# Kernel tuning notes

Measured on AMD Instinct MI355X. Metric: run time of the kernel, lower is better.

Reference implementation:

```python
import jax, jax.numpy as jnp
import numpy as np

N = 100000      # nodes
DEG = 16        # fixed degree
E = N * DEG     # edges
C_IN = 128
C_OUT = 128


def setup_inputs() -> dict:
    key = jax.random.key(0)
    k1, k2, k3, k4, k5 = jax.random.split(key, 5)
    x = jax.random.normal(k1, (N, C_IN), dtype=jnp.float32)
    # glorot-ish init for the dense weight
    scale = jnp.sqrt(6.0 / (C_IN + C_OUT)).astype(jnp.float32)
    weight = jax.random.uniform(k2, (C_IN, C_OUT), dtype=jnp.float32, minval=-1.0, maxval=1.0) * scale
    bias = jax.random.normal(k3, (C_OUT,), dtype=jnp.float32) * 0.02
    # fixed-degree CSR: every node has DEG in-edges; CSC analogously
    rowptr = (jnp.arange(N + 1, dtype=jnp.int32) * DEG)
    colind = jax.random.randint(k4, (E,), 0, N, dtype=jnp.int32)
    colptr = (jnp.arange(N + 1, dtype=jnp.int32) * DEG)
    rowind = jax.random.randint(k5, (E,), 0, N, dtype=jnp.int32)
    return {"x": x, "weight": weight, "bias": bias,
            "rowptr": rowptr, "colind": colind,
            "colptr": colptr, "rowind": rowind}


def _deg_inv_sqrt(indptr, dtype):
    deg = (indptr[1:] - indptr[:-1]).astype(dtype)
    return (1.0 / jnp.sqrt(deg))[:, None]  # [N, 1]


def reference(x, weight, bias, rowptr, colind, colptr, rowind):
    # dense transform: [N, C_in] @ [C_in, C_out]
    h = x @ weight
    in_norm = _deg_inv_sqrt(rowptr, h.dtype)    # 1/sqrt(in-degree)
    out_norm = _deg_inv_sqrt(colptr, h.dtype)   # 1/sqrt(out-degree)
    h = h * out_norm
    # CSR SpMM (unweighted): out[i] = sum_{e in [rowptr[i], rowptr[i+1])} h[colind[e]]
    n_nodes = rowptr.shape[0] - 1
    n_edges = colind.shape[0]
    row = jnp.searchsorted(rowptr, jnp.arange(n_edges, dtype=rowptr.dtype), side="right") - 1
    aggr = jax.ops.segment_sum(h[colind], row, num_segments=n_nodes)
    aggr = aggr * in_norm + bias
    return aggr
```

## Files before the change

### kernel.cpp

```cpp
#include <hip/hip_runtime.h>
#include <hip/hip_bf16.h>

#define N_NODES 100000
#define DEG 16
#define C 128
#define LDS_STRIDE 136

typedef __attribute__((ext_vector_type(8))) short short8;
typedef __attribute__((ext_vector_type(4))) float f32x4;

__device__ inline unsigned short f2bf(float f) {
    unsigned int u = __builtin_bit_cast(unsigned int, f);
    u += 0x7fffu + ((u >> 16) & 1u);
    return (unsigned short)(u >> 16);
}
__device__ inline float bflo(unsigned int p) { return __builtin_bit_cast(float, p << 16); }
__device__ inline float bfhi(unsigned int p) { return __builtin_bit_cast(float, p & 0xffff0000u); }

__global__ __launch_bounds__(256, 4)
void gcn_gemm_kernel(const float* __restrict__ x, const float* __restrict__ w,
                     const int* __restrict__ colptr, unsigned short* __restrict__ h)
{
    __shared__ unsigned short wt[C * LDS_STRIDE];

    int tid = threadIdx.x;
    for (int i = tid; i < C * C; i += 256) {
        int k = i >> 7;
        int n = i & 127;
        wt[n * LDS_STRIDE + k] = f2bf(w[i]);
    }
    __syncthreads();

    int wave = tid >> 6;
    int lane = tid & 63;
    int tile = blockIdx.x * 4 + wave;
    int m0 = tile * 16;
    if (m0 >= N_NODES) return;

    int lrow = lane & 15;
    int quad = lane >> 4;

    int gm_a = m0 + lrow;
    const float* xrow = x + (long)gm_a * C;
    short8 afrag[4];
#pragma unroll
    for (int kc = 0; kc < 4; ++kc) {
        int k0 = kc * 32 + quad * 8;
        f32x4 x0 = *reinterpret_cast<const f32x4*>(xrow + k0);
        f32x4 x1 = *reinterpret_cast<const f32x4*>(xrow + k0 + 4);
        short8 a;
        a[0] = (short)f2bf(x0[0]); a[1] = (short)f2bf(x0[1]);
        a[2] = (short)f2bf(x0[2]); a[3] = (short)f2bf(x0[3]);
        a[4] = (short)f2bf(x1[0]); a[5] = (short)f2bf(x1[1]);
        a[6] = (short)f2bf(x1[2]); a[7] = (short)f2bf(x1[3]);
        afrag[kc] = a;
    }

    float onorm[4];
#pragma unroll
    for (int r = 0; r < 4; ++r) {
        int gm = m0 + quad * 4 + r;
        onorm[r] = rsqrtf((float)(colptr[gm + 1] - colptr[gm]));
    }

#pragma unroll
    for (int nt = 0; nt < 8; ++nt) {
        f32x4 acc = {0.f, 0.f, 0.f, 0.f};
        int n = nt * 16 + lrow;
#pragma unroll
        for (int kc = 0; kc < 4; ++kc) {
            int k0 = kc * 32 + quad * 8;
            short8 b = *reinterpret_cast<const short8*>(&wt[n * LDS_STRIDE + k0]);
            acc = __builtin_amdgcn_mfma_f32_16x16x32_bf16(afrag[kc], b, acc, 0, 0, 0);
        }
#pragma unroll
        for (int r = 0; r < 4; ++r) {
            int gm = m0 + quad * 4 + r;
            h[(long)gm * C + nt * 16 + lrow] = f2bf(acc[r] * onorm[r]);
        }
    }
}

__global__ __launch_bounds__(256, 8)
void gcn_aggr_kernel(const unsigned short* __restrict__ h,
                     const int* __restrict__ rowptr,
                     const int* __restrict__ colind,
                     const float* __restrict__ bias,
                     float* __restrict__ out)
{
    int tid = threadIdx.x;
    int wave = tid >> 6;
    int lane = tid & 63;
    int node = blockIdx.x * 4 + wave;

    int cg = lane & 15;
    int eg = lane >> 4;

    int base = rowptr[node];
    int deg  = rowptr[node + 1] - base;
    float innorm = rsqrtf((float)deg);

    int myidx = colind[base + cg];

    float acc[8];
#pragma unroll
    for (int i = 0; i < 8; ++i) acc[i] = 0.f;

#pragma unroll
    for (int it = 0; it < 4; ++it) {
        int e = it * 4 + eg;
        int j = __shfl(myidx, e);
        const unsigned short* row = h + (long)j * C + cg * 8;
        int4 v = *reinterpret_cast<const int4*>(row);
        unsigned int p0 = (unsigned int)v.x;
        unsigned int p1 = (unsigned int)v.y;
        unsigned int p2 = (unsigned int)v.z;
        unsigned int p3 = (unsigned int)v.w;
        acc[0] += bflo(p0); acc[1] += bfhi(p0);
        acc[2] += bflo(p1); acc[3] += bfhi(p1);
        acc[4] += bflo(p2); acc[5] += bfhi(p2);
        acc[6] += bflo(p3); acc[7] += bfhi(p3);
    }

#pragma unroll
    for (int i = 0; i < 8; ++i) {
        acc[i] += __shfl_xor(acc[i], 16);
        acc[i] += __shfl_xor(acc[i], 32);
    }

    if (eg == 0) {
        const f32x4* bp = reinterpret_cast<const f32x4*>(bias + cg * 8);
        f32x4 b0 = bp[0], b1 = bp[1];
        f32x4 o0, o1;
        o0[0] = acc[0] * innorm + b0[0];
        o0[1] = acc[1] * innorm + b0[1];
        o0[2] = acc[2] * innorm + b0[2];
        o0[3] = acc[3] * innorm + b0[3];
        o1[0] = acc[4] * innorm + b1[0];
        o1[1] = acc[5] * innorm + b1[1];
        o1[2] = acc[6] * innorm + b1[2];
        o1[3] = acc[7] * innorm + b1[3];
        float* op = out + (long)node * C + cg * 8;
        *reinterpret_cast<f32x4*>(op)     = o0;
        *reinterpret_cast<f32x4*>(op + 4) = o1;
    }
}

extern "C" void kernel_launch(void* const* d_in, const int* in_sizes, int n_in,
                              void* d_out, int out_size, void* d_ws, size_t ws_size,
                              hipStream_t stream) {
    const float* x      = (const float*)d_in[0];
    const float* w      = (const float*)d_in[1];
    const float* bias   = (const float*)d_in[2];
    const int*   rowptr = (const int*)d_in[3];
    const int*   colind = (const int*)d_in[4];
    const int*   colptr = (const int*)d_in[5];
    float* out = (float*)d_out;
    unsigned short* h = (unsigned short*)d_ws;

    gcn_gemm_kernel<<<1563, 256, 0, stream>>>(x, w, colptr, h);
    gcn_aggr_kernel<<<25000, 256, 0, stream>>>(h, rowptr, colind, bias, out);
}
```

Baseline: 175.9 us.

## Make GEMM persistent with register-resident weights and prefetch; batch two nodes per aggregation wave

The GEMM kernel becomes persistent: 256 blocks of 8 waves. Each block stores W in LDS in MFMA-fragment order, and each wave keeps all B fragments in registers. Every wave loops over row tiles and prefetches the next tile's x while doing the MFMAs on the current one. This removes the per-block weight conversion that the old version repeated across 1563 blocks, and overlaps loads with compute, at the cost of high register pressure (128 VGPRs for the B fragments). The aggregation kernel now handles two nodes per wave and issues all 8 gather loads before accumulating, to raise memory-level parallelism. Its launch-bounds occupancy hint drops from 8 to 6.

Result: no change. 174.6 us (-0.7%).

```diff
diff --git a/kernel.cpp b/kernel.cpp
--- a/kernel.cpp
+++ b/kernel.cpp
@@ -4,7 +4,9 @@
 #define N_NODES 100000
 #define DEG 16
 #define C 128
-#define LDS_STRIDE 136
+#define NTILES 6250
+#define GEMM_BLOCKS 256
+#define GEMM_WAVES 8
 
 typedef __attribute__((ext_vector_type(8))) short short8;
 typedef __attribute__((ext_vector_type(4))) float f32x4;
@@ -17,71 +19,95 @@
 __device__ inline float bflo(unsigned int p) { return __builtin_bit_cast(float, p << 16); }
 __device__ inline float bfhi(unsigned int p) { return __builtin_bit_cast(float, p & 0xffff0000u); }
 
-__global__ __launch_bounds__(256, 4)
+__global__ __launch_bounds__(512, 2)
 void gcn_gemm_kernel(const float* __restrict__ x, const float* __restrict__ w,
                      const int* __restrict__ colptr, unsigned short* __restrict__ h)
 {
-    __shared__ unsigned short wt[C * LDS_STRIDE];
+    __shared__ unsigned short wfrag[32 * 64 * 8];
 
     int tid = threadIdx.x;
-    for (int i = tid; i < C * C; i += 256) {
-        int k = i >> 7;
-        int n = i & 127;
-        wt[n * LDS_STRIDE + k] = f2bf(w[i]);
+    for (int i = tid; i < C * C; i += 512) {
+        int k = i >> 7, n = i & 127;
+        int nt = n >> 4, lr = n & 15;
+        int kc = k >> 5, quad = (k >> 3) & 3, j = k & 7;
+        wfrag[((((nt << 2) + kc) << 6) + (quad << 4) + lr) * 8 + j] = f2bf(w[i]);
     }
     __syncthreads();
 
     int wave = tid >> 6;
     int lane = tid & 63;
-    int tile = blockIdx.x * 4 + wave;
-    int m0 = tile * 16;
-    if (m0 >= N_NODES) return;
-
     int lrow = lane & 15;
     int quad = lane >> 4;
 
-    int gm_a = m0 + lrow;
-    const float* xrow = x + (long)gm_a * C;
-    short8 afrag[4];
-#pragma unroll
-    for (int kc = 0; kc < 4; ++kc) {
-        int k0 = kc * 32 + quad * 8;
-        f32x4 x0 = *reinterpret_cast<const f32x4*>(xrow + k0);
-        f32x4 x1 = *reinterpret_cast<const f32x4*>(xrow + k0 + 4);
-        short8 a;
-        a[0] = (short)f2bf(x0[0]); a[1] = (short)f2bf(x0[1]);
-        a[2] = (short)f2bf(x0[2]); a[3] = (short)f2bf(x0[3]);
-        a[4] = (short)f2bf(x1[0]); a[5] = (short)f2bf(x1[1]);
-        a[6] = (short)f2bf(x1[2]); a[7] = (short)f2bf(x1[3]);
-        afrag[kc] = a;
-    }
-
-    float onorm[4];
-#pragma unroll
-    for (int r = 0; r < 4; ++r) {
-        int gm = m0 + quad * 4 + r;
-        onorm[r] = rsqrtf((float)(colptr[gm + 1] - colptr[gm]));
-    }
-
-#pragma unroll
-    for (int nt = 0; nt < 8; ++nt) {
-        f32x4 acc = {0.f, 0.f, 0.f, 0.f};
-        int n = nt * 16 + lrow;
+    short8 bf[8][4];
+#pragma unroll
+    for (int nt = 0; nt < 8; ++nt)
+#pragma unroll
+        for (int kc = 0; kc < 4; ++kc)
+            bf[nt][kc] = *reinterpret_cast<const short8*>(
+                &wfrag[((((nt << 2) + kc) << 6) + lane) * 8]);
+
+    int tile = blockIdx.x * GEMM_WAVES + wave;
+    if (tile >= NTILES) return;
+    const int tstride = GEMM_BLOCKS * GEMM_WAVES;
+
+    f32x4 xb[8];
+    {
+        const float* xr = x + (long)(tile * 16 + lrow) * C + quad * 8;
 #pragma unroll
         for (int kc = 0; kc < 4; ++kc) {
-            int k0 = kc * 32 + quad * 8;
-            short8 b = *reinterpret_cast<const short8*>(&wt[n * LDS_STRIDE + k0]);
-            acc = __builtin_amdgcn_mfma_f32_16x16x32_bf16(afrag[kc], b, acc, 0, 0, 0);
-        }
+            xb[2*kc]   = *reinterpret_cast<const f32x4*>(xr + kc * 32);
+            xb[2*kc+1] = *reinterpret_cast<const f32x4*>(xr + kc * 32 + 4);
+        }
+    }
+
+    while (true) {
+        int m0 = tile * 16;
+        short8 af[4];
+#pragma unroll
+        for (int kc = 0; kc < 4; ++kc) {
+            short8 a;
+            a[0] = (short)f2bf(xb[2*kc][0]);   a[1] = (short)f2bf(xb[2*kc][1]);
+            a[2] = (short)f2bf(xb[2*kc][2]);   a[3] = (short)f2bf(xb[2*kc][3]);
+            a[4] = (short)f2bf(xb[2*kc+1][0]); a[5] = (short)f2bf(xb[2*kc+1][1]);
+            a[6] = (short)f2bf(xb[2*kc+1][2]); a[7] = (short)f2bf(xb[2*kc+1][3]);
+            af[kc] = a;
+        }
+        float onorm[4];
 #pragma unroll
         for (int r = 0; r < 4; ++r) {
             int gm = m0 + quad * 4 + r;
-            h[(long)gm * C + nt * 16 + lrow] = f2bf(acc[r] * onorm[r]);
-        }
-    }
-}
-
-__global__ __launch_bounds__(256, 8)
+            onorm[r] = rsqrtf((float)(colptr[gm + 1] - colptr[gm]));
+        }
+
+        int next = tile + tstride;
+        bool more = next < NTILES;
+        if (more) {
+            const float* xr = x + (long)(next * 16 + lrow) * C + quad * 8;
+#pragma unroll
+            for (int kc = 0; kc < 4; ++kc) {
+                xb[2*kc]   = *reinterpret_cast<const f32x4*>(xr + kc * 32);
+                xb[2*kc+1] = *reinterpret_cast<const f32x4*>(xr + kc * 32 + 4);
+            }
+        }
+
+#pragma unroll
+        for (int nt = 0; nt < 8; ++nt) {
+            f32x4 acc = {0.f, 0.f, 0.f, 0.f};
+#pragma unroll
+            for (int kc = 0; kc < 4; ++kc)
+                acc = __builtin_amdgcn_mfma_f32_16x16x32_bf16(af[kc], bf[nt][kc], acc, 0, 0, 0);
+            unsigned short* hp = h + (long)(m0 + quad * 4) * C + nt * 16 + lrow;
+#pragma unroll
+            for (int r = 0; r < 4; ++r)
+                hp[r * C] = f2bf(acc[r] * onorm[r]);
+        }
+        if (!more) break;
+        tile = next;
+    }
+}
+
+__global__ __launch_bounds__(256, 6)
 void gcn_aggr_kernel(const unsigned short* __restrict__ h,
                      const int* __restrict__ rowptr,
                      const int* __restrict__ colind,
@@ -91,56 +117,73 @@
     int tid = threadIdx.x;
     int wave = tid >> 6;
     int lane = tid & 63;
-    int node = blockIdx.x * 4 + wave;
+    int node0 = (blockIdx.x * 4 + wave) * 2;
+    int node1 = node0 + 1;
 
     int cg = lane & 15;
     int eg = lane >> 4;
 
-    int base = rowptr[node];
-    int deg  = rowptr[node + 1] - base;
-    float innorm = rsqrtf((float)deg);
-
-    int myidx = colind[base + cg];
-
-    float acc[8];
-#pragma unroll
-    for (int i = 0; i < 8; ++i) acc[i] = 0.f;
-
+    int base0 = rowptr[node0];
+    int deg0  = rowptr[node0 + 1] - base0;
+    int base1 = rowptr[node1];
+    int deg1  = rowptr[node1 + 1] - base1;
+    float innorm0 = rsqrtf((float)deg0);
+    float innorm1 = rsqrtf((float)deg1);
+
+    int myidx0 = colind[base0 + cg];
+    int myidx1 = colind[base1 + cg];
+
+    int4 v0[4], v1[4];
 #pragma unroll
     for (int it = 0; it < 4; ++it) {
         int e = it * 4 + eg;
-        int j = __shfl(myidx, e);
-        const unsigned short* row = h + (long)j * C + cg * 8;
-        int4 v = *reinterpret_cast<const int4*>(row);
-        unsigned int p0 = (unsigned int)v.x;
-        unsigned int p1 = (unsigned int)v.y;
-        unsigned int p2 = (unsigned int)v.z;
-        unsigned int p3 = (unsigned int)v.w;
-        acc[0] += bflo(p0); acc[1] += bfhi(p0);
-        acc[2] += bflo(p1); acc[3] += bfhi(p1);
-        acc[4] += bflo(p2); acc[5] += bfhi(p2);
-        acc[6] += bflo(p3); acc[7] += bfhi(p3);
+        int j0 = __shfl(myidx0, e);
+        int j1 = __shfl(myidx1, e);
+        v0[it] = *reinterpret_cast<const int4*>(h + (long)j0 * C + cg * 8);
+        v1[it] = *reinterpret_cast<const int4*>(h + (long)j1 * C + cg * 8);
+    }
+
+    float acc0[8], acc1[8];
+#pragma unroll
+    for (int i = 0; i < 8; ++i) { acc0[i] = 0.f; acc1[i] = 0.f; }
+
+#pragma unroll
+    for (int it = 0; it < 4; ++it) {
+        unsigned int p;
+        p = (unsigned int)v0[it].x; acc0[0] += bflo(p); acc0[1] += bfhi(p);
+        p = (unsigned int)v0[it].y; acc0[2] += bflo(p); acc0[3] += bfhi(p);
+        p = (unsigned int)v0[it].z; acc0[4] += bflo(p); acc0[5] += bfhi(p);
+        p = (unsigned int)v0[it].w; acc0[6] += bflo(p); acc0[7] += bfhi(p);
+        p = (unsigned int)v1[it].x; acc1[0] += bflo(p); acc1[1] += bfhi(p);
+        p = (unsigned int)v1[it].y; acc1[2] += bflo(p); acc1[3] += bfhi(p);
+        p = (unsigned int)v1[it].z; acc1[4] += bflo(p); acc1[5] += bfhi(p);
+        p = (unsigned int)v1[it].w; acc1[6] += bflo(p); acc1[7] += bfhi(p);
     }
 
 #pragma unroll
     for (int i = 0; i < 8; ++i) {
-        acc[i] += __shfl_xor(acc[i], 16);
-        acc[i] += __shfl_xor(acc[i], 32);
-    }
-
-    if (eg == 0) {
+        acc0[i] += __shfl_xor(acc0[i], 16);
+        acc0[i] += __shfl_xor(acc0[i], 32);
+        acc1[i] += __shfl_xor(acc1[i], 16);
+        acc1[i] += __shfl_xor(acc1[i], 32);
+    }
+
+    if (eg < 2) {
+        float inn = (eg == 0) ? innorm0 : innorm1;
+        int   nd  = (eg == 0) ? node0 : node1;
+        float* a  = (eg == 0) ? acc0 : acc1;
         const f32x4* bp = reinterpret_cast<const f32x4*>(bias + cg * 8);
         f32x4 b0 = bp[0], b1 = bp[1];
         f32x4 o0, o1;
-        o0[0] = acc[0] * innorm + b0[0];
-        o0[1] = acc[1] * innorm + b0[1];
-        o0[2] = acc[2] * innorm + b0[2];
-        o0[3] = acc[3] * innorm + b0[3];
-        o1[0] = acc[4] * innorm + b1[0];
-        o1[1] = acc[5] * innorm + b1[1];
-        o1[2] = acc[6] * innorm + b1[2];
-        o1[3] = acc[7] * innorm + b1[3];
-        float* op = out + (long)node * C + cg * 8;
+        o0[0] = a[0] * inn + b0[0];
+        o0[1] = a[1] * inn + b0[1];
+        o0[2] = a[2] * inn + b0[2];
+        o0[3] = a[3] * inn + b0[3];
+        o1[0] = a[4] * inn + b1[0];
+        o1[1] = a[5] * inn + b1[1];
+        o1[2] = a[6] * inn + b1[2];
+        o1[3] = a[7] * inn + b1[3];
+        float* op = out + (long)nd * C + cg * 8;
         *reinterpret_cast<f32x4*>(op)     = o0;
         *reinterpret_cast<f32x4*>(op + 4) = o1;
     }
@@ -158,6 +201,6 @@
     float* out = (float*)d_out;
     unsigned short* h = (unsigned short*)d_ws;
 
-    gcn_gemm_kernel<<<1563, 256, 0, stream>>>(x, w, colptr, h);
-    gcn_aggr_kernel<<<25000, 256, 0, stream>>>(h, rowptr, colind, bias, out);
-}
+    gcn_gemm_kernel<<<GEMM_BLOCKS, 512, 0, stream>>>(x, w, colptr, h);
+    gcn_aggr_kernel<<<12500, 256, 0, stream>>>(h, rowptr, colind, bias, out);
+}
```
